# Kernel optimization log

Measured on AMD Instinct MI355X. Metric: run time of the kernel, lower is better.

## Reference

```python
import jax, jax.numpy as jnp
import numpy as np


def setup_inputs() -> dict:
    key = jax.random.key(0)
    ks = jax.random.split(key, 6)
    B, N, D, A = 4, 512, 768, 128
    matrix = jax.random.normal(ks[0], (B, N, D), dtype=jnp.float32)
    mask = jax.random.randint(ks[1], (B, N, N, 1), 0, 2, dtype=jnp.int32)
    W1_w = jax.random.normal(ks[2], (D, A), dtype=jnp.float32) * (1.0 / np.sqrt(D))
    W1_b = jnp.zeros((A,), dtype=jnp.float32)
    W2_w = jax.random.normal(ks[3], (D, A), dtype=jnp.float32) * (1.0 / np.sqrt(D))
    W2_b = jnp.zeros((A,), dtype=jnp.float32)
    v_w = jax.random.normal(ks[4], (A, 1), dtype=jnp.float32) * (1.0 / np.sqrt(A))
    return {"matrix": matrix, "mask": mask, "W1_w": W1_w, "W1_b": W1_b,
            "W2_w": W2_w, "W2_b": W2_b, "v_w": v_w}


def reference(matrix, mask, W1_w, W1_b, W2_w, W2_b, v_w):
    # matrix: [B,N,D]; mask: [B,N,N,1]
    w1 = matrix @ W1_w + W1_b                     # [B,N,A] (query-side proj)
    w2 = matrix @ W2_w + W2_b                     # [B,N,A] (key-side proj)
    # pairwise additive scores: v . tanh(w1_i + w2_j) -> [B,N,N]
    pair = jnp.tanh(w1[:, :, None, :] + w2[:, None, :, :])  # [B,N,N,A]
    scores = jnp.einsum('bija,ao->bij', pair, v_w)           # [B,N,N]
    boolean_mask = mask[..., 0].astype(bool)                  # [B,N,N]
    neg = jnp.finfo(scores.dtype).min
    masked = jnp.where(boolean_mask, scores, neg)
    attn = jax.nn.softmax(masked, axis=-1)
    attn = jnp.where(jnp.isnan(attn), jnp.zeros((), attn.dtype), attn)
    return attn @ matrix                          # [B,N,D]
```

## Files before the change

### kernel.cpp

```cpp
#include <hip/hip_runtime.h>

#define B_ 4
#define N_ 512
#define D_ 768
#define A_ 128

typedef short bf16x8 __attribute__((ext_vector_type(8)));
typedef ushort u16x8 __attribute__((ext_vector_type(8)));
typedef ushort u16x4 __attribute__((ext_vector_type(4)));
typedef float f32x4 __attribute__((ext_vector_type(4)));

__device__ __forceinline__ ushort f2h(float x) {
  uint u = __builtin_bit_cast(uint, x);
  return (ushort)((u + 0x7fffu + ((u >> 16) & 1u)) >> 16);
}
__device__ __forceinline__ float h2f(ushort h) {
  uint u = ((uint)h) << 16;
  return __builtin_bit_cast(float, u);
}
__device__ __forceinline__ bf16x8 ld8(const ushort* p) {
  return *(const bf16x8*)p;
}
#define MFMA(a, b, c) __builtin_amdgcn_mfma_f32_16x16x32_bf16(a, b, c, 0, 0, 0)

__global__ __launch_bounds__(256) void k0_prep(
    const float* __restrict__ M, const float* __restrict__ W1,
    const float* __restrict__ W2, const float* __restrict__ vw,
    ushort* __restrict__ Mr_h, ushort* __restrict__ Mr_l,
    ushort* __restrict__ Mt_h, ushort* __restrict__ Mt_l,
    ushort* __restrict__ Wt_h, ushort* __restrict__ Wt_l,
    float* __restrict__ uvec) {
  __shared__ ushort lds_h[64][40];
  __shared__ ushort lds_l[64][40];
  const int t = threadIdx.x;
  const int bid = blockIdx.x;
  if (bid < 768) {
    const int dq = bid % 12;
    const int rest = bid / 12;
    const int d0 = dq * 64;
    const int n0 = (rest & 15) * 32;
    const int b = rest >> 4;
    const int n = t >> 3;
    const int dg = (t & 7) * 8;
    const size_t roff = ((size_t)(b * N_ + n0 + n)) * D_ + d0 + dg;
    const float4 v0 = *(const float4*)(M + roff);
    const float4 v1 = *(const float4*)(M + roff + 4);
    const float x[8] = {v0.x, v0.y, v0.z, v0.w, v1.x, v1.y, v1.z, v1.w};
    u16x8 vh, vl;
#pragma unroll
    for (int e = 0; e < 8; ++e) {
      ushort h = f2h(x[e]);
      ushort l = f2h(x[e] - h2f(h));
      vh[e] = h;
      vl[e] = l;
      lds_h[dg + e][n] = h;
      lds_l[dg + e][n] = l;
    }
    *(u16x8*)(Mr_h + roff) = vh;
    *(u16x8*)(Mr_l + roff) = vl;
    __syncthreads();
    const int dd = t >> 2;
    const int ng = (t & 3) * 8;
    const size_t toff = ((size_t)b * D_ + d0 + dd) * N_ + n0 + ng;
    *(u16x8*)(Mt_h + toff) = *(const u16x8*)(&lds_h[dd][ng]);
    *(u16x8*)(Mt_l + toff) = *(const u16x8*)(&lds_l[dd][ng]);
  } else {
    const int c = t;
    const int k0 = (bid - 768) * 8;
    const float* __restrict__ Wp = (c < A_) ? W1 : W2;
    const int cc = c & (A_ - 1);
    u16x8 vh, vl;
#pragma unroll
    for (int e = 0; e < 8; ++e) {
      float x = Wp[(size_t)(k0 + e) * A_ + cc];
      ushort h = f2h(x);
      vh[e] = h;
      vl[e] = f2h(x - h2f(h));
    }
    *(u16x8*)(Wt_h + (size_t)c * D_ + k0) = vh;
    *(u16x8*)(Wt_l + (size_t)c * D_ + k0) = vl;
    if (bid == 768 && c < A_) uvec[c] = -2.f * vw[c];
  }
}

__global__ __launch_bounds__(256) void k1_mfma(
    const ushort* __restrict__ Mr_h, const ushort* __restrict__ Mr_l,
    const ushort* __restrict__ Wt_h, const ushort* __restrict__ Wt_l,
    const float* __restrict__ b1, const float* __restrict__ b2,
    float* __restrict__ w1e, float* __restrict__ w2e) {
  __shared__ float l_red[4][32][33];
  const int t = threadIdx.x;
  const int l = t & 63;
  const int w = t >> 6;
  const int r = l & 15, g = l >> 4;
  const int row0 = blockIdx.x * 32;
  const int cb = blockIdx.y * 32;
  const int kbase = w * 192;
  const size_t oA = (size_t)(row0 + r) * D_ + kbase + g * 8;
  const size_t oA2 = oA + (size_t)16 * D_;
  const size_t oB = (size_t)(cb + r) * D_ + kbase + g * 8;
  const size_t oB2 = oB + (size_t)16 * D_;
  f32x4 acc[2][2] = {};
  bf16x8 A[2][4], Bv[2][4];
#define K1LOAD(s, k0)                                                        \
  A[s][0] = ld8(Mr_h + oA + (k0));  A[s][1] = ld8(Mr_h + oA2 + (k0));        \
  A[s][2] = ld8(Mr_l + oA + (k0));  A[s][3] = ld8(Mr_l + oA2 + (k0));        \
  Bv[s][0] = ld8(Wt_h + oB + (k0)); Bv[s][1] = ld8(Wt_h + oB2 + (k0));       \
  Bv[s][2] = ld8(Wt_l + oB + (k0)); Bv[s][3] = ld8(Wt_l + oB2 + (k0));
#define K1MM(s)                                                              \
  acc[0][0] = MFMA(A[s][0], Bv[s][0], acc[0][0]);                            \
  acc[0][0] = MFMA(A[s][0], Bv[s][2], acc[0][0]);                            \
  acc[0][0] = MFMA(A[s][2], Bv[s][0], acc[0][0]);                            \
  acc[0][1] = MFMA(A[s][0], Bv[s][1], acc[0][1]);                            \
  acc[0][1] = MFMA(A[s][0], Bv[s][3], acc[0][1]);                            \
  acc[0][1] = MFMA(A[s][2], Bv[s][1], acc[0][1]);                            \
  acc[1][0] = MFMA(A[s][1], Bv[s][0], acc[1][0]);                            \
  acc[1][0] = MFMA(A[s][1], Bv[s][2], acc[1][0]);                            \
  acc[1][0] = MFMA(A[s][3], Bv[s][0], acc[1][0]);                            \
  acc[1][1] = MFMA(A[s][1], Bv[s][1], acc[1][1]);                            \
  acc[1][1] = MFMA(A[s][1], Bv[s][3], acc[1][1]);                            \
  acc[1][1] = MFMA(A[s][3], Bv[s][1], acc[1][1]);
  K1LOAD(0, 0)
#pragma unroll
  for (int kt = 0; kt < 6; ++kt) {
    if (kt & 1) {
      if (kt < 5) { K1LOAD(0, (kt + 1) * 32) }
      K1MM(1)
    } else {
      if (kt < 5) { K1LOAD(1, (kt + 1) * 32) }
      K1MM(0)
    }
  }
#undef K1LOAD
#undef K1MM
#pragma unroll
  for (int fi = 0; fi < 2; ++fi)
#pragma unroll
    for (int fj = 0; fj < 2; ++fj)
#pragma unroll
      for (int rr = 0; rr < 4; ++rr)
        l_red[w][fi * 16 + g * 4 + rr][fj * 16 + r] = acc[fi][fj][rr];
  __syncthreads();

  const float SC = 2.8853900817779268f;
  const int b = row0 >> 9;
  const int n0 = row0 & (N_ - 1);
  if (cb < A_) {
#pragma unroll
    for (int k = 0; k < 4; ++k) {
      const int row = (t >> 5) + k * 8;
      const int col = t & 31;
      float v = l_red[0][row][col] + l_red[1][row][col] +
                l_red[2][row][col] + l_red[3][row][col];
      v = (v + b1[cb + col]) * SC;
      w1e[(size_t)(row0 + row) * A_ + cb + col] = __builtin_amdgcn_exp2f(v);
    }
  } else {
#pragma unroll
    for (int k = 0; k < 4; ++k) {
      const int row = t & 31;
      const int col = (t >> 5) + k * 8;
      float v = l_red[0][row][col] + l_red[1][row][col] +
                l_red[2][row][col] + l_red[3][row][col];
      v = (v + b2[cb - A_ + col]) * SC;
      w2e[(size_t)(b * A_ + cb - A_ + col) * N_ + n0 + row] =
          __builtin_amdgcn_exp2f(v);
    }
  }
}

__global__ __launch_bounds__(1024) void k2_scores(
    const float* __restrict__ w1e, const float* __restrict__ w2e,
    const float* __restrict__ uvec, const int* __restrict__ mask,
    const float* __restrict__ vw, ushort* __restrict__ ah,
    ushort* __restrict__ al) {
  __shared__ float l_w2[2][16][N_];
  __shared__ float l_red[8][2];
  __shared__ float l_sum[8][2];
  const int t = threadIdx.x;
  const int lane = t & 63;
  const int w = t >> 6;
  const int r = w >> 1;
  const int h = w & 1;
  const int i0 = blockIdx.x * 8;
  const int b = i0 >> 9;
  const int i = i0 + r;
  const int iu = __builtin_amdgcn_readfirstlane(i);
  const float* __restrict__ w1row = w1e + (size_t)iu * A_;

  float vs = vw[lane] + vw[64 + lane];
#pragma unroll
  for (int off = 32; off; off >>= 1) vs += __shfl_xor(vs, off);

  const float* __restrict__ w2src = w2e + (size_t)b * A_ * N_;
  float4 st[2];

#define STAGE_LOAD(cc)                                                      \
  {                                                                         \
    const float* __restrict__ src = w2src + (size_t)(cc) * 16 * N_;         \
    _Pragma("unroll") for (int k = 0; k < 2; ++k) {                         \
      const int f = t + k * 1024;                                           \
      st[k] = *(const float4*)(src + (size_t)(f >> 7) * N_ + (f & 127) * 4);\
    }                                                                       \
  }
#define STAGE_WRITE(bf)                                                     \
  {                                                                         \
    _Pragma("unroll") for (int k = 0; k < 2; ++k) {                         \
      const int f = t + k * 1024;                                           \
      *(float4*)(&l_w2[bf][f >> 7][(f & 127) * 4]) = st[k];                 \
    }                                                                       \
  }

  STAGE_LOAD(0)
  STAGE_WRITE(0)
  __syncthreads();

  const int jb = h * 256 + lane * 4;
  float4 s = {0.f, 0.f, 0.f, 0.f};
#pragma unroll 1
  for (int cc = 0; cc < 8; ++cc) {
    if (cc + 1 < 8) STAGE_LOAD(cc + 1)
    const float(*wb)[N_] = l_w2[cc & 1];
#pragma unroll 1
    for (int aa = 0; aa < 4; ++aa) {
      const float4 wa = *(const float4*)(w1row + cc * 16 + aa * 4);
      const float4 uu = *(const float4*)(uvec + cc * 16 + aa * 4);
      const float wa_[4] = {wa.x, wa.y, wa.z, wa.w};
      const float uu_[4] = {uu.x, uu.y, uu.z, uu.w};
#pragma unroll
      for (int e = 0; e < 4; ++e) {
        const float wx = wa_[e];
        const float ux = uu_[e];
        const float4 x = *(const float4*)(&wb[aa * 4 + e][jb]);
        s.x = fmaf(ux, __builtin_amdgcn_rcpf(fmaf(wx, x.x, 1.f)), s.x);
        s.y = fmaf(ux, __builtin_amdgcn_rcpf(fmaf(wx, x.y, 1.f)), s.y);
        s.z = fmaf(ux, __builtin_amdgcn_rcpf(fmaf(wx, x.z, 1.f)), s.z);
        s.w = fmaf(ux, __builtin_amdgcn_rcpf(fmaf(wx, x.w, 1.f)), s.w);
      }
    }
    if (cc + 1 < 8) { STAGE_WRITE((cc + 1) & 1) }
    __syncthreads();
  }
#undef STAGE_LOAD
#undef STAGE_WRITE

  const float NEG = -3.402823466e38f;
  const int4 mk = *(const int4*)(mask + (size_t)i * N_ + jb);
  s.x = mk.x ? (vs + s.x) : NEG;
  s.y = mk.y ? (vs + s.y) : NEG;
  s.z = mk.z ? (vs + s.z) : NEG;
  s.w = mk.w ? (vs + s.w) : NEG;

  float rmax = fmaxf(fmaxf(s.x, s.y), fmaxf(s.z, s.w));
#pragma unroll
  for (int off = 32; off; off >>= 1) rmax = fmaxf(rmax, __shfl_xor(rmax, off));
  if (lane == 0) l_red[r][h] = rmax;
  __syncthreads();
  rmax = fmaxf(l_red[r][0], l_red[r][1]);

  const float L2E = 1.4426950408889634f;
  s.x = __builtin_amdgcn_exp2f((s.x - rmax) * L2E);
  s.y = __builtin_amdgcn_exp2f((s.y - rmax) * L2E);
  s.z = __builtin_amdgcn_exp2f((s.z - rmax) * L2E);
  s.w = __builtin_amdgcn_exp2f((s.w - rmax) * L2E);
  float psum = (s.x + s.y) + (s.z + s.w);
#pragma unroll
  for (int off = 32; off; off >>= 1) psum += __shfl_xor(psum, off);
  if (lane == 0) l_sum[r][h] = psum;
  __syncthreads();
  const float inv = __builtin_amdgcn_rcpf(l_sum[r][0] + l_sum[r][1]);

  const float p[4] = {s.x * inv, s.y * inv, s.z * inv, s.w * inv};
  u16x4 vh, vl;
#pragma unroll
  for (int e = 0; e < 4; ++e) {
    const ushort hh = f2h(p[e]);
    vh[e] = hh;
    vl[e] = f2h(p[e] - h2f(hh));
  }
  *(u16x4*)(ah + (size_t)i * N_ + jb) = vh;
  *(u16x4*)(al + (size_t)i * N_ + jb) = vl;
}

__global__ __launch_bounds__(256) void k3_mfma(
    const ushort* __restrict__ ah, const ushort* __restrict__ al,
    const ushort* __restrict__ Mt_h, const ushort* __restrict__ Mt_l,
    float* __restrict__ out) {
  __shared__ float l_red[4][64][33];
  const int t = threadIdx.x;
  const int l = t & 63;
  const int w = t >> 6;
  const int r = l & 15, g = l >> 4;
  const int row0 = blockIdx.x * 64;
  const int d0 = blockIdx.y * 32;
  const int b = row0 >> 9;
  const int jbase = w * 128;
  const ushort* __restrict__ Bh = Mt_h + (size_t)b * D_ * N_;
  const ushort* __restrict__ Bl = Mt_l + (size_t)b * D_ * N_;
  size_t oA[4];
#pragma unroll
  for (int fi = 0; fi < 4; ++fi)
    oA[fi] = (size_t)(row0 + fi * 16 + r) * N_ + jbase + g * 8;
  const size_t oB = (size_t)(d0 + r) * N_ + jbase + g * 8;
  const size_t oB2 = oB + (size_t)16 * N_;
  f32x4 acc[4][2] = {};
  bf16x8 A[2][8], Bv[2][4];
#define K3LOAD(s, j0)                                                        \
  A[s][0] = ld8(ah + oA[0] + (j0)); A[s][1] = ld8(ah + oA[1] + (j0));        \
  A[s][2] = ld8(ah + oA[2] + (j0)); A[s][3] = ld8(ah + oA[3] + (j0));        \
  A[s][4] = ld8(al + oA[0] + (j0)); A[s][5] = ld8(al + oA[1] + (j0));        \
  A[s][6] = ld8(al + oA[2] + (j0)); A[s][7] = ld8(al + oA[3] + (j0));        \
  Bv[s][0] = ld8(Bh + oB + (j0));   Bv[s][1] = ld8(Bh + oB2 + (j0));         \
  Bv[s][2] = ld8(Bl + oB + (j0));   Bv[s][3] = ld8(Bl + oB2 + (j0));
#define K3MM(s)                                                              \
  _Pragma("unroll") for (int fi = 0; fi < 4; ++fi)                           \
  _Pragma("unroll") for (int fd = 0; fd < 2; ++fd) {                         \
    acc[fi][fd] = MFMA(A[s][fi], Bv[s][fd], acc[fi][fd]);                    \
    acc[fi][fd] = MFMA(A[s][fi], Bv[s][fd + 2], acc[fi][fd]);                \
    acc[fi][fd] = MFMA(A[s][fi + 4], Bv[s][fd], acc[fi][fd]);                \
  }
  K3LOAD(0, 0)
#pragma unroll
  for (int kt = 0; kt < 4; ++kt) {
    if (kt & 1) {
      if (kt < 3) { K3LOAD(0, (kt + 1) * 32) }
      K3MM(1)
    } else {
      if (kt < 3) { K3LOAD(1, (kt + 1) * 32) }
      K3MM(0)
    }
  }
#undef K3LOAD
#undef K3MM
#pragma unroll
  for (int fi = 0; fi < 4; ++fi)
#pragma unroll
    for (int fd = 0; fd < 2; ++fd)
#pragma unroll
      for (int rr = 0; rr < 4; ++rr)
        l_red[w][fi * 16 + g * 4 + rr][fd * 16 + r] = acc[fi][fd][rr];
  __syncthreads();
#pragma unroll
  for (int k = 0; k < 8; ++k) {
    const int row = (t >> 5) + k * 8;
    const int col = t & 31;
    const float v = l_red[0][row][col] + l_red[1][row][col] +
                    l_red[2][row][col] + l_red[3][row][col];
    out[(size_t)(row0 + row) * D_ + d0 + col] = v;
  }
}

extern "C" void kernel_launch(void* const* d_in, const int* in_sizes, int n_in,
                              void* d_out, int out_size, void* d_ws,
                              size_t ws_size, hipStream_t stream) {
  const float* M = (const float*)d_in[0];
  const int* mask = (const int*)d_in[1];
  const float* W1 = (const float*)d_in[2];
  const float* b1 = (const float*)d_in[3];
  const float* W2 = (const float*)d_in[4];
  const float* b2 = (const float*)d_in[5];
  const float* vw = (const float*)d_in[6];
  float* out = (float*)d_out;

  float* w1e = (float*)d_ws;
  float* w2e = w1e + 2048 * A_;
  ushort* ah = (ushort*)(w2e + 4 * A_ * N_);
  ushort* al = ah + 2048 * N_;
  ushort* Mr_h = al + 2048 * N_;
  ushort* Mr_l = Mr_h + 2048 * D_;
  ushort* Mt_h = Mr_l + 2048 * D_;
  ushort* Mt_l = Mt_h + 2048 * D_;
  ushort* Wt_h = Mt_l + 2048 * D_;
  ushort* Wt_l = Wt_h + 256 * D_;
  float* uvec = (float*)(Wt_l + 256 * D_);

  k0_prep<<<864, 256, 0, stream>>>(M, W1, W2, vw, Mr_h, Mr_l, Mt_h, Mt_l,
                                   Wt_h, Wt_l, uvec);
  k1_mfma<<<dim3(2048 / 32, 8), 256, 0, stream>>>(Mr_h, Mr_l, Wt_h, Wt_l,
                                                  b1, b2, w1e, w2e);
  k2_scores<<<(B_ * N_) / 8, 1024, 0, stream>>>(w1e, w2e, uvec, mask, vw,
                                                ah, al);
  k3_mfma<<<dim3(2048 / 64, D_ / 32), 256, 0, stream>>>(ah, al, Mt_h, Mt_l,
                                                        out);
}
```

Baseline: 69.95 us.

## Store exp(w2) as bf16 and shrink score blocks to four rows

The exponentiated key-side projection is now written by the projection kernel as bf16 instead of fp32. The scores kernel stages it into shared memory at half the size and widens it back to float before the reciprocal/FMA accumulation. The scores kernel also moves from 1024-thread blocks covering 8 query rows to 512-thread blocks covering 4 rows, which halves per-block LDS and doubles the grid. This cuts global and LDS traffic for w2e, at the cost of bf16 rounding on the exponentials feeding the tanh score, which may affect accuracy.

```diff
diff --git a/kernel.cpp b/kernel.cpp
--- a/kernel.cpp
+++ b/kernel.cpp
@@ -87,7 +87,7 @@
     const ushort* __restrict__ Mr_h, const ushort* __restrict__ Mr_l,
     const ushort* __restrict__ Wt_h, const ushort* __restrict__ Wt_l,
     const float* __restrict__ b1, const float* __restrict__ b2,
-    float* __restrict__ w1e, float* __restrict__ w2e) {
+    float* __restrict__ w1e, ushort* __restrict__ w2e) {
   __shared__ float l_red[4][32][33];
   const int t = threadIdx.x;
   const int l = t & 63;
@@ -164,25 +164,25 @@
                 l_red[2][row][col] + l_red[3][row][col];
       v = (v + b2[cb - A_ + col]) * SC;
       w2e[(size_t)(b * A_ + cb - A_ + col) * N_ + n0 + row] =
-          __builtin_amdgcn_exp2f(v);
-    }
-  }
-}
-
-__global__ __launch_bounds__(1024) void k2_scores(
-    const float* __restrict__ w1e, const float* __restrict__ w2e,
+          f2h(__builtin_amdgcn_exp2f(v));
+    }
+  }
+}
+
+__global__ __launch_bounds__(512) void k2_scores(
+    const float* __restrict__ w1e, const ushort* __restrict__ w2e,
     const float* __restrict__ uvec, const int* __restrict__ mask,
     const float* __restrict__ vw, ushort* __restrict__ ah,
     ushort* __restrict__ al) {
-  __shared__ float l_w2[2][16][N_];
-  __shared__ float l_red[8][2];
-  __shared__ float l_sum[8][2];
+  __shared__ ushort l_w2[2][16][N_];
+  __shared__ float l_red[4][2];
+  __shared__ float l_sum[4][2];
   const int t = threadIdx.x;
   const int lane = t & 63;
   const int w = t >> 6;
   const int r = w >> 1;
   const int h = w & 1;
-  const int i0 = blockIdx.x * 8;
+  const int i0 = blockIdx.x * 4;
   const int b = i0 >> 9;
   const int i = i0 + r;
   const int iu = __builtin_amdgcn_readfirstlane(i);
@@ -192,22 +192,22 @@
 #pragma unroll
   for (int off = 32; off; off >>= 1) vs += __shfl_xor(vs, off);
 
-  const float* __restrict__ w2src = w2e + (size_t)b * A_ * N_;
-  float4 st[2];
+  const ushort* __restrict__ w2src = w2e + (size_t)b * A_ * N_;
+  u16x8 st[2];
 
 #define STAGE_LOAD(cc)                                                      \
   {                                                                         \
-    const float* __restrict__ src = w2src + (size_t)(cc) * 16 * N_;         \
+    const ushort* __restrict__ src = w2src + (size_t)(cc) * 16 * N_;        \
     _Pragma("unroll") for (int k = 0; k < 2; ++k) {                         \
-      const int f = t + k * 1024;                                           \
-      st[k] = *(const float4*)(src + (size_t)(f >> 7) * N_ + (f & 127) * 4);\
+      const int f = t + k * 512;                                            \
+      st[k] = *(const u16x8*)(src + (size_t)(f >> 6) * N_ + (f & 63) * 8);  \
     }                                                                       \
   }
 #define STAGE_WRITE(bf)                                                     \
   {                                                                         \
     _Pragma("unroll") for (int k = 0; k < 2; ++k) {                         \
-      const int f = t + k * 1024;                                           \
-      *(float4*)(&l_w2[bf][f >> 7][(f & 127) * 4]) = st[k];                 \
+      const int f = t + k * 512;                                            \
+      *(u16x8*)(&l_w2[bf][f >> 6][(f & 63) * 8]) = st[k];                   \
     }                                                                       \
   }
 
@@ -220,7 +220,7 @@
 #pragma unroll 1
   for (int cc = 0; cc < 8; ++cc) {
     if (cc + 1 < 8) STAGE_LOAD(cc + 1)
-    const float(*wb)[N_] = l_w2[cc & 1];
+    const ushort(*wb)[N_] = l_w2[cc & 1];
 #pragma unroll 1
     for (int aa = 0; aa < 4; ++aa) {
       const float4 wa = *(const float4*)(w1row + cc * 16 + aa * 4);
@@ -231,11 +231,11 @@
       for (int e = 0; e < 4; ++e) {
         const float wx = wa_[e];
         const float ux = uu_[e];
-        const float4 x = *(const float4*)(&wb[aa * 4 + e][jb]);
-        s.x = fmaf(ux, __builtin_amdgcn_rcpf(fmaf(wx, x.x, 1.f)), s.x);
-        s.y = fmaf(ux, __builtin_amdgcn_rcpf(fmaf(wx, x.y, 1.f)), s.y);
-        s.z = fmaf(ux, __builtin_amdgcn_rcpf(fmaf(wx, x.z, 1.f)), s.z);
-        s.w = fmaf(ux, __builtin_amdgcn_rcpf(fmaf(wx, x.w, 1.f)), s.w);
+        const u16x4 xr = *(const u16x4*)(&wb[aa * 4 + e][jb]);
+        s.x = fmaf(ux, __builtin_amdgcn_rcpf(fmaf(wx, h2f(xr[0]), 1.f)), s.x);
+        s.y = fmaf(ux, __builtin_amdgcn_rcpf(fmaf(wx, h2f(xr[1]), 1.f)), s.y);
+        s.z = fmaf(ux, __builtin_amdgcn_rcpf(fmaf(wx, h2f(xr[2]), 1.f)), s.z);
+        s.w = fmaf(ux, __builtin_amdgcn_rcpf(fmaf(wx, h2f(xr[3]), 1.f)), s.w);
       }
     }
     if (cc + 1 < 8) { STAGE_WRITE((cc + 1) & 1) }
@@ -363,8 +363,8 @@
   float* out = (float*)d_out;
 
   float* w1e = (float*)d_ws;
-  float* w2e = w1e + 2048 * A_;
-  ushort* ah = (ushort*)(w2e + 4 * A_ * N_);
+  ushort* w2eb = (ushort*)(w1e + 2048 * A_);
+  ushort* ah = w2eb + 4 * A_ * N_;
   ushort* al = ah + 2048 * N_;
   ushort* Mr_h = al + 2048 * N_;
   ushort* Mr_l = Mr_h + 2048 * D_;
@@ -377,9 +377,9 @@
   k0_prep<<<864, 256, 0, stream>>>(M, W1, W2, vw, Mr_h, Mr_l, Mt_h, Mt_l,
                                    Wt_h, Wt_l, uvec);
   k1_mfma<<<dim3(2048 / 32, 8), 256, 0, stream>>>(Mr_h, Mr_l, Wt_h, Wt_l,
-                                                  b1, b2, w1e, w2e);
-  k2_scores<<<(B_ * N_) / 8, 1024, 0, stream>>>(w1e, w2e, uvec, mask, vw,
-                                                ah, al);
+                                                  b1, b2, w1e, w2eb);
+  k2_scores<<<(B_ * N_) / 4, 512, 0, stream>>>(w1e, w2eb, uvec, mask, vw,
+                                               ah, al);
   k3_mfma<<<dim3(2048 / 64, D_ / 32), 256, 0, stream>>>(ah, al, Mt_h, Mt_l,
                                                         out);
 }
```

Result: faster. 66.99 us (-4.2%).
